# Kernel optimization log

Hardware: AMD Instinct MI355X
Metric: run time of the kernel (lower is better)

## Reference

```python
import jax, jax.numpy as jnp
import numpy as np

D = 256          # common_dim = specific_dim
NH = 8           # num_heads
HD = D // NH     # head_dim = 32
B, S = 16, 1024
EPS = 1e-5


def _mha(q, k, v, wq, bq, wk, bk, wv, bv, wo, bo):
    # q,k,v: [B, S, D]; weights stored [in, out] so y = x @ w + b
    b_, _, _ = q.shape

    def proj(x, w, b):
        return (x @ w + b).reshape(b_, -1, NH, HD).transpose(0, 2, 1, 3)  # [B,H,S,hd]

    Q, K, V = proj(q, wq, bq), proj(k, wk, bk), proj(v, wv, bv)
    scores = jnp.einsum('bhqd,bhkd->bhqk', Q, K) / (float(HD) ** 0.5)
    attn = jax.nn.softmax(scores, axis=-1)
    out = jnp.einsum('bhqk,bhkd->bhqd', attn, V)
    out = out.transpose(0, 2, 1, 3).reshape(b_, -1, D)
    return out @ wo + bo


def _ln(x, g, b):
    mu = jnp.mean(x, axis=-1, keepdims=True)
    var = jnp.var(x, axis=-1, keepdims=True)
    return (x - mu) * jax.lax.rsqrt(var + EPS) * g + b


def setup_inputs() -> dict:
    key = jax.random.key(0)
    ks = iter(jax.random.split(key, 32))
    rn = lambda *shape: jax.random.normal(next(ks), shape, dtype=jnp.float32)
    w = lambda i, o: rn(i, o) * 0.05
    inp = {
        'img_common': rn(B, S, D),
        'txt_common': rn(B, S, D),
        'img_specific': rn(B, D),
        'txt_specific': rn(B, D),
    }
    for pfx in ('i2t', 't2i'):
        for nm in ('q', 'k', 'v', 'o'):
            inp[f'{pfx}_w{nm}'] = w(D, D)
            inp[f'{pfx}_b{nm}'] = jnp.zeros((D,), jnp.float32)
    inp['ln_img_g'] = jnp.ones((D,), jnp.float32)
    inp['ln_img_b'] = jnp.zeros((D,), jnp.float32)
    inp['ln_txt_g'] = jnp.ones((D,), jnp.float32)
    inp['ln_txt_b'] = jnp.zeros((D,), jnp.float32)
    inp['enh_w'] = w(2 * D, D)
    inp['enh_b'] = jnp.zeros((D,), jnp.float32)
    inp['inc_w'] = w(2 * D, D)
    inp['inc_b'] = jnp.zeros((D,), jnp.float32)
    return inp


def reference(img_common, txt_common, img_specific, txt_specific,
              i2t_wq, i2t_bq, i2t_wk, i2t_bk, i2t_wv, i2t_bv, i2t_wo, i2t_bo,
              t2i_wq, t2i_bq, t2i_wk, t2i_bk, t2i_wv, t2i_bv, t2i_wo, t2i_bo,
              ln_img_g, ln_img_b, ln_txt_g, ln_txt_b,
              enh_w, enh_b, inc_w, inc_b):
    att_i2t = _mha(img_common, txt_common, txt_common,
                   i2t_wq, i2t_bq, i2t_wk, i2t_bk, i2t_wv, i2t_bv, i2t_wo, i2t_bo)
    img_query = _ln(att_i2t + img_common, ln_img_g, ln_img_b)
    att_t2i = _mha(txt_common, img_common, img_common,
                   t2i_wq, t2i_bq, t2i_wk, t2i_bk, t2i_wv, t2i_bv, t2i_wo, t2i_bo)
    txt_query = _ln(att_t2i + txt_common, ln_txt_g, ln_txt_b)
    combined = jnp.concatenate((img_query, txt_query), axis=-1)  # [B,S,2D]
    enhancement = combined @ enh_w + enh_b                        # [B,S,D]
    inc = jnp.concatenate((img_specific - txt_specific,
                           img_specific * txt_specific), axis=1)  # [B,2D]
    inconsistency = inc @ inc_w + inc_b                           # [B,D]
    return (enhancement, inconsistency, img_specific, txt_specific)
```

## Files before the change

kernel.cpp:

```cpp
#include <hip/hip_runtime.h>
#include <stdint.h>

typedef unsigned int u32;
typedef unsigned short u16;
typedef __attribute__((ext_vector_type(8))) short bf16x8;
typedef __attribute__((ext_vector_type(4))) float f32x4;

#define BUF_ELEMS (16384 * 256)

__device__ __forceinline__ float bflo(u32 u) { return __uint_as_float(u << 16); }
__device__ __forceinline__ float bfhi(u32 u) { return __uint_as_float(u & 0xffff0000u); }
__device__ __forceinline__ u16 f2bf(float f) {
    u32 u = __float_as_uint(f);
    return (u16)((u + 0x7fffu + ((u >> 16) & 1u)) >> 16);
}
__device__ __forceinline__ u32 pkhi(float lo, float hi) {
    return __builtin_amdgcn_perm(__float_as_uint(hi), __float_as_uint(lo), 0x07060302u);
}
__device__ __forceinline__ float fexp2(float x) {
#if __has_builtin(__builtin_amdgcn_exp2f)
    return __builtin_amdgcn_exp2f(x);
#else
    float r; asm("v_exp_f32 %0, %1" : "=v"(r) : "v"(x)); return r;
#endif
}
__device__ __forceinline__ float frcp(float x) {
#if __has_builtin(__builtin_amdgcn_rcpf)
    return __builtin_amdgcn_rcpf(x);
#else
    return 1.f / x;
#endif
}

struct WT {
    const float* src[9];
    u16* dst[9];
    const float* bs[6];
    float* bA;
    float* bB;
    const float* img_sp;
    const float* txt_sp;
    const float* incw;
    const float* incb;
    float* out_inc;
    float* out_img;
    float* out_txt;
};

__global__ __launch_bounds__(256)
void wtrans_kernel(WT wt)
{
    __shared__ float T[64][65];
    const int bid = blockIdx.x, t = threadIdx.x;
    if (bid == 160) {
        wt.bA[t]       = wt.bs[0][t];
        wt.bA[256 + t] = wt.bs[1][t];
        wt.bA[512 + t] = wt.bs[2][t];
        wt.bB[t]       = wt.bs[3][t];
        wt.bB[256 + t] = wt.bs[4][t];
        wt.bB[512 + t] = wt.bs[5][t];
        return;
    }
    if (bid > 160) {
        float* iv = &T[0][0];
        const int b = bid - 161, n = t;
        float a = wt.img_sp[b * 256 + n];
        float x = wt.txt_sp[b * 256 + n];
        iv[n] = a - x;
        iv[256 + n] = a * x;
        __syncthreads();
        float acc = wt.incb[n];
        for (int k = 0; k < 512; k++) acc += iv[k] * wt.incw[k * 256 + n];
        wt.out_inc[b * 256 + n] = acc;
        wt.out_img[b * 256 + n] = a;
        wt.out_txt[b * 256 + n] = x;
        return;
    }
    int m, sub;
    if (bid < 128) { m = bid >> 4; sub = bid & 15; }
    else           { m = 8;        sub = bid - 128; }
    const int K = (m == 8) ? 512 : 256;
    const int kt = (m == 8) ? (sub & 7) : (sub & 3);
    const int nt = (m == 8) ? (sub >> 3) : (sub >> 2);
    const int k0 = kt * 64, n0 = nt * 64;
    const float* src = wt.src[m];
    u16* dst = wt.dst[m];

    const int kk = t >> 2, nn = (t & 3) * 16;
    #pragma unroll
    for (int j = 0; j < 16; j += 4) {
        float4 v = *(const float4*)(src + (size_t)(k0 + kk) * 256 + n0 + nn + j);
        T[kk][nn + j + 0] = v.x; T[kk][nn + j + 1] = v.y;
        T[kk][nn + j + 2] = v.z; T[kk][nn + j + 3] = v.w;
    }
    __syncthreads();
    const int nn2 = t >> 2, kc = (t & 3) * 16;
    #pragma unroll
    for (int j = 0; j < 16; j++)
        dst[(size_t)(n0 + nn2) * K + k0 + kc + j] = f2bf(T[kc + j][nn2]);
}

template<int MODE>
__global__ __launch_bounds__(256)
void gemm_mfma(const float* __restrict__ Af0, const float* __restrict__ Af1,
               const u16* __restrict__ Ab0, const u16* __restrict__ Ab1,
               const u16* __restrict__ Wt0, const u16* __restrict__ Wt1,
               const float* __restrict__ bias0, const float* __restrict__ bias1,
               void* __restrict__ o0, void* __restrict__ o1, void* __restrict__ o2,
               void* __restrict__ o3, void* __restrict__ o4, void* __restrict__ o5)
{
    __shared__ u16 As[128][72];
    __shared__ u16 Bs[128][72];
    const int tid = threadIdx.x;
    const int wave = tid >> 6, lane = tid & 63;
    const int L = lane & 15, Qd = lane >> 4;
    int m_idx, n_idx;
    if (MODE == 0)      { m_idx = blockIdx.x & 255; n_idx = blockIdx.x >> 8; }
    else if (MODE == 1) { m_idx = blockIdx.x & 255; n_idx = blockIdx.x >> 8; }
    else                { m_idx = blockIdx.x & 127; n_idx = blockIdx.x >> 7; }
    const bool ms = (MODE == 0 || MODE == 1) ? (m_idx >= 128) : false;
    const int lm0 = (MODE == 2) ? m_idx * 128 : (m_idx & 127) * 128;
    const int n0 = n_idx * 128;
    const u16* Wt = ms ? Wt1 : Wt0;
    const float* bias = ms ? bias1 : bias0;
    const int wr = wave & 1, wc = wave >> 1;
    const int sr = tid >> 1, sh = (tid & 1) * 32;
    const int KS = (MODE == 2) ? 512 : 256;

    f32x4 acc[4][4] = {};

    for (int kt = 0; kt < KS; kt += 64) {
        if (MODE == 0) {
            const float* Af = ms ? Af1 : Af0;
            const float* Ap = Af + (size_t)(lm0 + sr) * 256 + kt + sh;
            uint4 pk[2];
            #pragma unroll
            for (int half = 0; half < 2; half++) {
                float4 f0 = *(const float4*)(Ap + half * 16);
                float4 f1 = *(const float4*)(Ap + half * 16 + 4);
                float4 f2 = *(const float4*)(Ap + half * 16 + 8);
                float4 f3 = *(const float4*)(Ap + half * 16 + 12);
                pk[half].x = pkhi(f0.x, f0.y);
                pk[half].y = pkhi(f0.z, f0.w);
                pk[half].z = pkhi(f1.x, f1.y);
                pk[half].w = pkhi(f1.z, f1.w);
                uint4 q;
                q.x = pkhi(f2.x, f2.y); q.y = pkhi(f2.z, f2.w);
                q.z = pkhi(f3.x, f3.y); q.w = pkhi(f3.z, f3.w);
                *(uint4*)&As[sr][sh + half * 16 + 8] = q;
            }
            *(uint4*)&As[sr][sh + 0] = pk[0];
            *(uint4*)&As[sr][sh + 16] = pk[1];
        } else {
            const u16* Abase;
            int lkt = kt;
            if (MODE == 2) { Abase = (kt < 256) ? Ab0 : Ab1; lkt = kt & 255; }
            else           { Abase = ms ? Ab1 : Ab0; }
            const u16* Ap = Abase + (size_t)(lm0 + sr) * 256 + lkt + sh;
            uint4 a0 = *(const uint4*)(Ap + 0);
            uint4 a1 = *(const uint4*)(Ap + 8);
            uint4 a2 = *(const uint4*)(Ap + 16);
            uint4 a3 = *(const uint4*)(Ap + 24);
            *(uint4*)&As[sr][sh + 0]  = a0;
            *(uint4*)&As[sr][sh + 8]  = a1;
            *(uint4*)&As[sr][sh + 16] = a2;
            *(uint4*)&As[sr][sh + 24] = a3;
        }
        {
            const u16* Bp = Wt + (size_t)(n0 + sr) * KS + kt + sh;
            uint4 w0 = *(const uint4*)(Bp + 0);
            uint4 w1 = *(const uint4*)(Bp + 8);
            uint4 w2 = *(const uint4*)(Bp + 16);
            uint4 w3 = *(const uint4*)(Bp + 24);
            *(uint4*)&Bs[sr][sh + 0]  = w0;
            *(uint4*)&Bs[sr][sh + 8]  = w1;
            *(uint4*)&Bs[sr][sh + 16] = w2;
            *(uint4*)&Bs[sr][sh + 24] = w3;
        }
        __syncthreads();
        #pragma unroll
        for (int kh = 0; kh < 64; kh += 32) {
            bf16x8 af[4], bf[4];
            #pragma unroll
            for (int mt = 0; mt < 4; mt++)
                af[mt] = *(const bf16x8*)&As[wr * 64 + mt * 16 + L][kh + Qd * 8];
            #pragma unroll
            for (int nt = 0; nt < 4; nt++)
                bf[nt] = *(const bf16x8*)&Bs[wc * 64 + nt * 16 + L][kh + Qd * 8];
            #pragma unroll
            for (int mt = 0; mt < 4; mt++)
                #pragma unroll
                for (int nt = 0; nt < 4; nt++)
                    acc[mt][nt] = __builtin_amdgcn_mfma_f32_16x16x32_bf16(
                        af[mt], bf[nt], acc[mt][nt], 0, 0, 0);
        }
        __syncthreads();
    }

    float bvals[4];
    #pragma unroll
    for (int nt = 0; nt < 4; nt++)
        bvals[nt] = bias[n0 + wc * 64 + nt * 16 + L];

    const float qsc = (MODE == 0 && n_idx < 2)
                      ? (0.17677669529663687f * 1.4426950408889634f) : 1.0f;

    void* outp;
    int colb;
    if (MODE == 0) {
        const int g = n_idx >> 1;
        if (!ms) outp = (g == 0) ? o0 : ((g == 1) ? o1 : o2);
        else     outp = (g == 0) ? o3 : ((g == 1) ? o4 : o5);
        colb = (n_idx & 1) * 128 + wc * 64;
    } else if (MODE == 1) {
        outp = ms ? o1 : o0;
        colb = n0 + wc * 64;
    } else {
        outp = o0;
        colb = n0 + wc * 64;
    }

    if (MODE == 0 && n_idx >= 4) {
        u16* Vg = (u16*)outp;
        #pragma unroll
        for (int mt = 0; mt < 4; mt++) {
            const int tokb = lm0 + wr * 64 + mt * 16 + Qd * 4;
            const int b_ = tokb >> 10;
            const int s_ = tokb & 1023;
            #pragma unroll
            for (int nt = 0; nt < 4; nt++) {
                const int col = colb + nt * 16 + L;
                const int h_ = col >> 5, d_ = col & 31;
                uint2 pk2;
                pk2.x = (u32)f2bf(acc[mt][nt][0] + bvals[nt])
                      | ((u32)f2bf(acc[mt][nt][1] + bvals[nt]) << 16);
                pk2.y = (u32)f2bf(acc[mt][nt][2] + bvals[nt])
                      | ((u32)f2bf(acc[mt][nt][3] + bvals[nt]) << 16);
                *(uint2*)(Vg + ((size_t)((b_ * 8 + h_) * 32 + d_) << 10) + s_) = pk2;
            }
        }
        return;
    }

    #pragma unroll
    for (int mt = 0; mt < 4; mt++) {
        #pragma unroll
        for (int r = 0; r < 4; r++) {
            const size_t row = (size_t)(lm0 + wr * 64 + mt * 16 + Qd * 4 + r) * 256;
            #pragma unroll
            for (int nt = 0; nt < 4; nt++) {
                const int col = colb + nt * 16 + L;
                float v = (acc[mt][nt][r] + bvals[nt]) * qsc;
                if (MODE == 2) ((float*)outp)[row + col] = v;
                else           ((u16*)outp)[row + col] = f2bf(v);
            }
        }
    }
}

__global__ __launch_bounds__(256, 4)
void attn_mfma(const u16* __restrict__ Q0, const u16* __restrict__ K0,
               const u16* __restrict__ V0, u16* __restrict__ O0,
               const u16* __restrict__ Q1, const u16* __restrict__ K1,
               const u16* __restrict__ V1, u16* __restrict__ O1)
{
    __shared__ u16 Ks[128][40];
    __shared__ u16 Vt[32][136];
    __shared__ u16 Ps[4][16][136];
    const int tid = threadIdx.x;
    const int wave = tid >> 6, lane = tid & 63;
    const int L = lane & 15, Qd = lane >> 4;
    const int bid = blockIdx.x;
    const int qt = (bid >> 3) & 7;
    const int kv = (bid & 7) | ((bid >> 6) << 3);
    const int set = kv >> 7;
    const int b = (kv >> 3) & 15;
    const int h = kv & 7;
    const u16* Q = set ? Q1 : Q0;
    const u16* K = set ? K1 : K0;
    const u16* V = set ? V1 : V0;
    u16* O = set ? O1 : O0;
    const int rowbase = b * 1024;
    const int qbase = rowbase + qt * 128;

    bf16x8 qfrag[2];
    #pragma unroll
    for (int qs = 0; qs < 2; qs++)
        qfrag[qs] = *(const bf16x8*)(Q + (size_t)(qbase + qs * 64 + wave * 16 + L) * 256
                                       + h * 32 + Qd * 8);

    const short oneb = (short)0x3F80;
    const bf16x8 ones = {oneb, oneb, oneb, oneb, oneb, oneb, oneb, oneb};

    f32x4 oacc[2][2] = {};
    f32x4 oaccL[2] = {};

    const int kkey  = ((tid >> 4) & 7) | (((tid >> 1) & 7) << 3) | ((tid >> 7) << 6);
    const int kcolh = (tid & 1) * 16;
    const int krow  = (kkey & 7) * 16 + (kkey >> 3);
    const int vd    = tid >> 3;
    const int vkb   = (tid & 7) * 16;
    const size_t vplane = (size_t)((b * 8 + h) * 32 + vd) * 1024;

    uint4 kr0, kr1, vr0, vr1;
    {
        const size_t kb = (size_t)(rowbase + kkey) * 256 + h * 32 + kcolh;
        kr0 = *(const uint4*)(K + kb);
        kr1 = *(const uint4*)(K + kb + 8);
        const size_t vb = vplane + vkb;
        vr0 = *(const uint4*)(V + vb);
        vr1 = *(const uint4*)(V + vb + 8);
    }

    for (int t = 0; t < 8; t++) {
        *(uint4*)&Ks[krow][kcolh]     = kr0;
        *(uint4*)&Ks[krow][kcolh + 8] = kr1;
        *(uint4*)&Vt[vd][vkb]         = vr0;
        *(uint4*)&Vt[vd][vkb + 8]     = vr1;
        __syncthreads();

        if (t < 7) {
            const size_t kb = (size_t)(rowbase + (t + 1) * 128 + kkey) * 256 + h * 32 + kcolh;
            kr0 = *(const uint4*)(K + kb);
            kr1 = *(const uint4*)(K + kb + 8);
            const size_t vb = vplane + (t + 1) * 128 + vkb;
            vr0 = *(const uint4*)(V + vb);
            vr1 = *(const uint4*)(V + vb + 8);
        }

        bf16x8 kf[8];
        #pragma unroll
        for (int ct = 0; ct < 8; ct++)
            kf[ct] = *(const bf16x8*)&Ks[ct * 16 + L][Qd * 8];

        bf16x8 vfr[4][2];
        #pragma unroll
        for (int kc = 0; kc < 4; kc++) {
            vfr[kc][0] = *(const bf16x8*)&Vt[L][kc * 32 + Qd * 8];
            vfr[kc][1] = *(const bf16x8*)&Vt[16 + L][kc * 32 + Qd * 8];
        }

        #pragma unroll
        for (int qs = 0; qs < 2; qs++) {
            const f32x4 z = {0.f, 0.f, 0.f, 0.f};
            f32x4 sacc[8];
            #pragma unroll
            for (int ct = 0; ct < 8; ct++)
                sacc[ct] = __builtin_amdgcn_mfma_f32_16x16x32_bf16(qfrag[qs], kf[ct], z, 0, 0, 0);
            #pragma unroll
            for (int r = 0; r < 4; r++) {
                float p[8];
                #pragma unroll
                for (int ct = 0; ct < 8; ct++) p[ct] = fexp2(sacc[ct][r]);
                uint4 pk;
                pk.x = pkhi(p[0], p[1]);
                pk.y = pkhi(p[2], p[3]);
                pk.z = pkhi(p[4], p[5]);
                pk.w = pkhi(p[6], p[7]);
                *(uint4*)&Ps[wave][Qd * 4 + r][L * 8] = pk;
            }
            #pragma unroll
            for (int kc = 0; kc < 4; kc++) {
                bf16x8 pfrag = *(const bf16x8*)&Ps[wave][L][kc * 32 + Qd * 8];
                oacc[qs][0] = __builtin_amdgcn_mfma_f32_16x16x32_bf16(pfrag, vfr[kc][0], oacc[qs][0], 0, 0, 0);
                oacc[qs][1] = __builtin_amdgcn_mfma_f32_16x16x32_bf16(pfrag, vfr[kc][1], oacc[qs][1], 0, 0, 0);
                oaccL[qs]   = __builtin_amdgcn_mfma_f32_16x16x32_bf16(pfrag, ones, oaccL[qs], 0, 0, 0);
            }
        }
        __syncthreads();
    }

    #pragma unroll
    for (int qs = 0; qs < 2; qs++) {
        #pragma unroll
        for (int r = 0; r < 4; r++) {
            float inv = frcp(oaccL[qs][r]);
            const size_t orow = (size_t)(qbase + qs * 64 + wave * 16 + Qd * 4 + r) * 256 + h * 32;
            O[orow + L]      = f2bf(oacc[qs][0][r] * inv);
            O[orow + 16 + L] = f2bf(oacc[qs][1][r] * inv);
        }
    }
}

__global__ __launch_bounds__(256)
void ln_res_kernel(const u16* __restrict__ P0, const u16* __restrict__ P1,
                   const float* __restrict__ R0, const float* __restrict__ R1,
                   const float* __restrict__ g0, const float* __restrict__ be0,
                   const float* __restrict__ g1, const float* __restrict__ be1,
                   u16* __restrict__ out0, u16* __restrict__ out1)
{
    const int lane = threadIdx.x & 63;
    int row = blockIdx.x * 4 + (threadIdx.x >> 6);
    const bool sel = row >= 16384;
    const u16* P = sel ? P1 : P0;
    const float* R = sel ? R1 : R0;
    const float* g = sel ? g1 : g0;
    const float* be = sel ? be1 : be0;
    u16* out = sel ? out1 : out0;
    if (sel) row -= 16384;
    const int col = lane * 4;
    uint2 pv = *(const uint2*)(P + (size_t)row * 256 + col);
    float4 rv = *(const float4*)(R + (size_t)row * 256 + col);
    float x0 = bflo(pv.x) + rv.x;
    float x1 = bfhi(pv.x) + rv.y;
    float x2 = bflo(pv.y) + rv.z;
    float x3 = bfhi(pv.y) + rv.w;
    float s = x0 + x1 + x2 + x3;
    float s2 = x0*x0 + x1*x1 + x2*x2 + x3*x3;
    #pragma unroll
    for (int off = 32; off > 0; off >>= 1) {
        s  += __shfl_xor(s, off);
        s2 += __shfl_xor(s2, off);
    }
    float mean = s * 0.00390625f;
    float var = fmaxf(s2 * 0.00390625f - mean * mean, 0.f);
    float rstd = rsqrtf(var + 1e-5f);
    float4 gv = *(const float4*)(g + col);
    float4 bv = *(const float4*)(be + col);
    uint2 pk;
    pk.x = (u32)f2bf((x0 - mean) * rstd * gv.x + bv.x)
         | ((u32)f2bf((x1 - mean) * rstd * gv.y + bv.y) << 16);
    pk.y = (u32)f2bf((x2 - mean) * rstd * gv.z + bv.z)
         | ((u32)f2bf((x3 - mean) * rstd * gv.w + bv.w) << 16);
    *(uint2*)(out + (size_t)row * 256 + col) = pk;
}

extern "C" void kernel_launch(void* const* d_in, const int* in_sizes, int n_in,
                              void* d_out, int out_size, void* d_ws, size_t ws_size,
                              hipStream_t stream)
{
    (void)in_sizes; (void)n_in; (void)out_size; (void)ws_size;
    const float* img    = (const float*)d_in[0];
    const float* txt    = (const float*)d_in[1];
    const float* img_sp = (const float*)d_in[2];
    const float* txt_sp = (const float*)d_in[3];
    const float* wq_i = (const float*)d_in[4];  const float* bq_i = (const float*)d_in[5];
    const float* wk_i = (const float*)d_in[6];  const float* bk_i = (const float*)d_in[7];
    const float* wv_i = (const float*)d_in[8];  const float* bv_i = (const float*)d_in[9];
    const float* wo_i = (const float*)d_in[10]; const float* bo_i = (const float*)d_in[11];
    const float* wq_t = (const float*)d_in[12]; const float* bq_t = (const float*)d_in[13];
    const float* wk_t = (const float*)d_in[14]; const float* bk_t = (const float*)d_in[15];
    const float* wv_t = (const float*)d_in[16]; const float* bv_t = (const float*)d_in[17];
    const float* wo_t = (const float*)d_in[18]; const float* bo_t = (const float*)d_in[19];
    const float* lng_i = (const float*)d_in[20]; const float* lnb_i = (const float*)d_in[21];
    const float* lng_t = (const float*)d_in[22]; const float* lnb_t = (const float*)d_in[23];
    const float* enh_w = (const float*)d_in[24]; const float* enh_b = (const float*)d_in[25];
    const float* incw  = (const float*)d_in[26]; const float* incb  = (const float*)d_in[27];
    float* out = (float*)d_out;
    u16* wsp = (u16*)d_ws;
    u16* B0 = wsp;
    u16* B1 = wsp + 1 * (size_t)BUF_ELEMS;
    u16* B2 = wsp + 2 * (size_t)BUF_ELEMS;
    u16* B3 = wsp + 3 * (size_t)BUF_ELEMS;
    u16* B4 = wsp + 4 * (size_t)BUF_ELEMS;
    u16* B5 = wsp + 5 * (size_t)BUF_ELEMS;
    u16* wbase = wsp + 6 * (size_t)BUF_ELEMS;
    u16* WtA   = wbase;
    u16* WtB   = wbase + 196608;
    u16* Wt_oi = wbase + 393216;
    u16* Wt_ot = wbase + 458752;
    u16* Wt_en = wbase + 524288;
    float* biasA = (float*)(wbase + 655360);
    float* biasB = biasA + 768;

    dim3 blk(256);
    WT wt;
    wt.src[0] = wq_i; wt.dst[0] = WtA;
    wt.src[1] = wk_t; wt.dst[1] = WtA + 65536;
    wt.src[2] = wv_t; wt.dst[2] = WtA + 131072;
    wt.src[3] = wq_t; wt.dst[3] = WtB;
    wt.src[4] = wk_i; wt.dst[4] = WtB + 65536;
    wt.src[5] = wv_i; wt.dst[5] = WtB + 131072;
    wt.src[6] = wo_i; wt.dst[6] = Wt_oi;
    wt.src[7] = wo_t; wt.dst[7] = Wt_ot;
    wt.src[8] = enh_w; wt.dst[8] = Wt_en;
    wt.bs[0] = bq_i; wt.bs[1] = bk_t; wt.bs[2] = bv_t;
    wt.bs[3] = bq_t; wt.bs[4] = bk_i; wt.bs[5] = bv_i;
    wt.bA = biasA; wt.bB = biasB;
    wt.img_sp = img_sp; wt.txt_sp = txt_sp; wt.incw = incw; wt.incb = incb;
    wt.out_inc = out + 4194304; wt.out_img = out + 4198400; wt.out_txt = out + 4202496;
    wtrans_kernel<<<177, blk, 0, stream>>>(wt);

    gemm_mfma<0><<<1536, blk, 0, stream>>>(img, txt, nullptr, nullptr,
                                           WtA, WtB, biasA, biasB,
                                           B0, B4, B5, B3, B1, B2);
    attn_mfma<<<2048, blk, 0, stream>>>(B0, B1, B2, B0, B3, B4, B5, B3);
    gemm_mfma<1><<<512, blk, 0, stream>>>(nullptr, nullptr, B0, B3,
                                          Wt_oi, Wt_ot, bo_i, bo_t,
                                          B1, B4, nullptr, nullptr, nullptr, nullptr);
    ln_res_kernel<<<8192, blk, 0, stream>>>(B1, B4, img, txt,
                                            lng_i, lnb_i, lng_t, lnb_t, B2, B5);
    gemm_mfma<2><<<256, blk, 0, stream>>>(nullptr, nullptr, B2, B5,
                                          Wt_en, nullptr, enh_b, nullptr,
                                          out, nullptr, nullptr, nullptr, nullptr, nullptr);
}
```

Baseline: 272.1 us.

## Keep softmax probabilities in registers via transposed S^T MFMA in attention

The attention kernel now computes S^T = K·Q^T so each lane's MFMA output directly forms the B-operand fragment for the P·V product. The LDS round trip through the Ps buffer is gone, and the K rows are permuted in shared memory so the register layout matches. The output accumulator is transposed too, which lets the final store write packed 4-element bf16 chunks per lane. This removes LDS writes and reads plus their latency and cuts LDS footprint, which may raise occupancy. It relies on an intricate key permutation being correct.

```diff
diff --git a/kernel.cpp b/kernel.cpp
--- a/kernel.cpp
+++ b/kernel.cpp
@@ -266,7 +266,6 @@
 {
     __shared__ u16 Ks[128][40];
     __shared__ u16 Vt[32][136];
-    __shared__ u16 Ps[4][16][136];
     const int tid = threadIdx.x;
     const int wave = tid >> 6, lane = tid & 63;
     const int L = lane & 15, Qd = lane >> 4;
@@ -292,12 +291,15 @@
     const short oneb = (short)0x3F80;
     const bf16x8 ones = {oneb, oneb, oneb, oneb, oneb, oneb, oneb, oneb};
 
-    f32x4 oacc[2][2] = {};
+    f32x4 oaccT[2][2] = {};
     f32x4 oaccL[2] = {};
 
-    const int kkey  = ((tid >> 4) & 7) | (((tid >> 1) & 7) << 3) | ((tid >> 7) << 6);
+    const int s     = tid >> 1;
+    const int kkey  = (s & 3) | (((s >> 3) & 1) << 2) | (((s >> 2) & 1) << 3)
+                    | (((s >> 4) & 1) << 4) | ((s >> 5) << 5);
     const int kcolh = (tid & 1) * 16;
-    const int krow  = (kkey & 7) * 16 + (kkey >> 3);
+    const int krow  = (kkey & 96) | (((kkey >> 2) & 1) << 4)
+                    | (((kkey >> 3) & 3) << 2) | (kkey & 3);
     const int vd    = tid >> 3;
     const int vkb   = (tid & 7) * 16;
     const size_t vplane = (size_t)((b * 8 + h) * 32 + vd) * 1024;
@@ -343,41 +345,35 @@
         #pragma unroll
         for (int qs = 0; qs < 2; qs++) {
             const f32x4 z = {0.f, 0.f, 0.f, 0.f};
-            f32x4 sacc[8];
-            #pragma unroll
-            for (int ct = 0; ct < 8; ct++)
-                sacc[ct] = __builtin_amdgcn_mfma_f32_16x16x32_bf16(qfrag[qs], kf[ct], z, 0, 0, 0);
-            #pragma unroll
-            for (int r = 0; r < 4; r++) {
-                float p[8];
-                #pragma unroll
-                for (int ct = 0; ct < 8; ct++) p[ct] = fexp2(sacc[ct][r]);
-                uint4 pk;
-                pk.x = pkhi(p[0], p[1]);
-                pk.y = pkhi(p[2], p[3]);
-                pk.z = pkhi(p[4], p[5]);
-                pk.w = pkhi(p[6], p[7]);
-                *(uint4*)&Ps[wave][Qd * 4 + r][L * 8] = pk;
+            #pragma unroll
+            for (int kc = 0; kc < 4; kc++) {
+                f32x4 s0 = __builtin_amdgcn_mfma_f32_16x16x32_bf16(kf[2 * kc],     qfrag[qs], z, 0, 0, 0);
+                f32x4 s1 = __builtin_amdgcn_mfma_f32_16x16x32_bf16(kf[2 * kc + 1], qfrag[qs], z, 0, 0, 0);
+                union { u32 w[4]; bf16x8 v; } pf;
+                pf.w[0] = pkhi(fexp2(s0[0]), fexp2(s0[1]));
+                pf.w[1] = pkhi(fexp2(s0[2]), fexp2(s0[3]));
+                pf.w[2] = pkhi(fexp2(s1[0]), fexp2(s1[1]));
+                pf.w[3] = pkhi(fexp2(s1[2]), fexp2(s1[3]));
+                oaccT[qs][0] = __builtin_amdgcn_mfma_f32_16x16x32_bf16(vfr[kc][0], pf.v, oaccT[qs][0], 0, 0, 0);
+                oaccT[qs][1] = __builtin_amdgcn_mfma_f32_16x16x32_bf16(vfr[kc][1], pf.v, oaccT[qs][1], 0, 0, 0);
+                oaccL[qs]    = __builtin_amdgcn_mfma_f32_16x16x32_bf16(ones,       pf.v, oaccL[qs],    0, 0, 0);
             }
-            #pragma unroll
-            for (int kc = 0; kc < 4; kc++) {
-                bf16x8 pfrag = *(const bf16x8*)&Ps[wave][L][kc * 32 + Qd * 8];
-                oacc[qs][0] = __builtin_amdgcn_mfma_f32_16x16x32_bf16(pfrag, vfr[kc][0], oacc[qs][0], 0, 0, 0);
-                oacc[qs][1] = __builtin_amdgcn_mfma_f32_16x16x32_bf16(pfrag, vfr[kc][1], oacc[qs][1], 0, 0, 0);
-                oaccL[qs]   = __builtin_amdgcn_mfma_f32_16x16x32_bf16(pfrag, ones, oaccL[qs], 0, 0, 0);
-            }
         }
         __syncthreads();
     }
 
     #pragma unroll
     for (int qs = 0; qs < 2; qs++) {
-        #pragma unroll
-        for (int r = 0; r < 4; r++) {
-            float inv = frcp(oaccL[qs][r]);
-            const size_t orow = (size_t)(qbase + qs * 64 + wave * 16 + Qd * 4 + r) * 256 + h * 32;
-            O[orow + L]      = f2bf(oacc[qs][0][r] * inv);
-            O[orow + 16 + L] = f2bf(oacc[qs][1][r] * inv);
+        float inv = frcp(oaccL[qs][0]);
+        u16* op = O + (size_t)(qbase + qs * 64 + wave * 16 + L) * 256 + h * 32 + Qd * 4;
+        #pragma unroll
+        for (int db = 0; db < 2; db++) {
+            uint2 w;
+            w.x = (u32)f2bf(oaccT[qs][db][0] * inv)
+                | ((u32)f2bf(oaccT[qs][db][1] * inv) << 16);
+            w.y = (u32)f2bf(oaccT[qs][db][2] * inv)
+                | ((u32)f2bf(oaccT[qs][db][3] * inv) << 16);
+            *(uint2*)(op + db * 16) = w;
         }
     }
 }
```

Result: faster. 264.4 us (-2.8%).
